# Kernel tuning notes

Measured on AMD Instinct MI355X. Metric: run time of the kernel, lower is better.

Reference implementation:

```python
import jax, jax.numpy as jnp
import numpy as np

N_QUBITS = 8

# Quantum circuit math: starting from |0...0>, apply RX(x_i) then RY(theta_i) on each
# wire independently (product state preserved). Exact PauliZ expectation per wire:
#   RX(x)|0> = cos(x/2)|0> - i sin(x/2)|1>;  after RY(t):
#   <Z> = cos(x) * cos(t)
# This is the exact closed form of the full state-vector simulation the torch module runs.

def setup_inputs() -> dict:
    key = jax.random.key(0)
    k1, k2, k3, k4 = jax.random.split(key, 4)
    B, S, D, F = 4, 4096, 1024, 4096
    x = jax.random.normal(k1, (B, S, D), dtype=jnp.float32)
    theta = jax.random.normal(k2, (N_QUBITS,), dtype=jnp.float32)
    W1 = jax.random.normal(k3, (F, N_QUBITS), dtype=jnp.float32) * (1.0 / np.sqrt(N_QUBITS))
    W2 = jax.random.normal(k4, (D, F), dtype=jnp.float32) * (1.0 / np.sqrt(F))
    return {"x": x, "theta": theta, "W1": W1, "W2": W2}


def reference(x, theta, W1, W2):
    # Encoder only reads the first n_qubits features of each token.
    z = jnp.cos(x[..., :N_QUBITS]) * jnp.cos(theta)          # [B, S, Q] PauliZ expectations
    h = jax.nn.relu(jnp.einsum('bsq,fq->bsf', z, W1))        # [B, S, ffn_dim]
    return jnp.einsum('bsf,df->bsd', h, W2)                  # [B, S, embed_dim]
```

## Files before the change

### kernel.cpp

```cpp
#include <hip/hip_runtime.h>
#include <hip/hip_bf16.h>
#include <math.h>


using f32x4  = __attribute__((ext_vector_type(4))) float;
using bf16x8 = __attribute__((ext_vector_type(8))) short;
using i32x4  = __attribute__((ext_vector_type(4))) int;

#define M_TOT 16384
#define N_TOT 1024
#define K_TOT 4096
#define NKT   128
#define ATB   16384
#define BTB   8192

static const size_t H_BYTES   = (size_t)M_TOT * K_TOT * 2;
static const size_t W2B_BYTES = (size_t)N_TOT * K_TOT * 2;
static const size_t WS_NEED   = H_BYTES + W2B_BYTES;

#define SWZ32(row, bytecol) ((bytecol) ^ ((((row) >> 1) & 3) << 4))

#define GLD16(gp, lp) __builtin_amdgcn_global_load_lds( \
    (const __attribute__((address_space(1))) unsigned int*)(const void*)(gp), \
    (__attribute__((address_space(3))) unsigned int*)(void*)(lp), 16, 0, 0)

static __device__ inline unsigned short f2bf(float f) {
    __hip_bfloat16 b = __float2bfloat16(f);
    unsigned short u;
    __builtin_memcpy(&u, &b, 2);
    return u;
}

__global__ __launch_bounds__(256)
void k_prep(const float* __restrict__ x, const float* __restrict__ theta,
            const float* __restrict__ W1, const float* __restrict__ W2,
            char* __restrict__ hws, char* __restrict__ w2ws)
{
    __shared__ float sZ[256 * 8];
    __shared__ float sW[128 * 8];
    const int tid = threadIdx.x;

    if (blockIdx.x < 2048) {
        const int bx = blockIdx.x >> 5;
        const int by = blockIdx.x & 31;

        {
            const float* xp = x + ((size_t)bx * 256 + tid) * 1024;
            f32x4 a = *reinterpret_cast<const f32x4*>(xp);
            f32x4 b = *reinterpret_cast<const f32x4*>(xp + 4);
            #pragma unroll
            for (int q = 0; q < 4; ++q) {
                sZ[tid * 8 + q]     = cosf(a[q]) * cosf(theta[q]);
                sZ[tid * 8 + 4 + q] = cosf(b[q]) * cosf(theta[q + 4]);
            }
        }
        *reinterpret_cast<f32x4*>(&sW[tid * 4]) =
            *reinterpret_cast<const f32x4*>(W1 + (size_t)by * 1024 + tid * 4);
        __syncthreads();

        const int tm = tid >> 4;
        const int tk = tid & 15;

        f32x4 wA[8], wB[8];
        #pragma unroll
        for (int kk = 0; kk < 8; ++kk) {
            wA[kk] = *reinterpret_cast<const f32x4*>(&sW[(tk * 8 + kk) * 8]);
            wB[kk] = *reinterpret_cast<const f32x4*>(&sW[(tk * 8 + kk) * 8 + 4]);
        }

        const int kt = by * 4 + (tk >> 2);
        const int slotb = (tk & 3) * 16;
        char* tb = hws + ((size_t)(bx * NKT + kt)) * ATB;

        #pragma unroll
        for (int i = 0; i < 16; ++i) {
            const int R = tm * 16 + i;
            f32x4 za = *reinterpret_cast<const f32x4*>(&sZ[R * 8]);
            f32x4 zb = *reinterpret_cast<const f32x4*>(&sZ[R * 8 + 4]);
            unsigned hu[8];
            #pragma unroll
            for (int kk = 0; kk < 8; ++kk) {
                float h = 0.f;
                #pragma unroll
                for (int q = 0; q < 4; ++q) {
                    h = fmaf(za[q], wA[kk][q], h);
                    h = fmaf(zb[q], wB[kk][q], h);
                }
                hu[kk] = (unsigned)f2bf(fmaxf(h, 0.f));
            }
            i32x4 pk;
            pk[0] = (int)(hu[0] | (hu[1] << 16));
            pk[1] = (int)(hu[2] | (hu[3] << 16));
            pk[2] = (int)(hu[4] | (hu[5] << 16));
            pk[3] = (int)(hu[6] | (hu[7] << 16));
            *reinterpret_cast<i32x4*>(tb + R * 64 + SWZ32(R, slotb)) = pk;
        }
    } else {
        const int gt = (blockIdx.x - 2048) * 256 + tid;
        const int n  = gt >> 9;
        const int k8 = gt & 511;
        const float* p = W2 + (size_t)n * K_TOT + k8 * 8;
        f32x4 a = *reinterpret_cast<const f32x4*>(p);
        f32x4 b = *reinterpret_cast<const f32x4*>(p + 4);
        i32x4 pk;
        pk[0] = (int)((unsigned)f2bf(a[0]) | ((unsigned)f2bf(a[1]) << 16));
        pk[1] = (int)((unsigned)f2bf(a[2]) | ((unsigned)f2bf(a[3]) << 16));
        pk[2] = (int)((unsigned)f2bf(b[0]) | ((unsigned)f2bf(b[1]) << 16));
        pk[3] = (int)((unsigned)f2bf(b[2]) | ((unsigned)f2bf(b[3]) << 16));
        const int nt = n >> 7, r = n & 127, kt = k8 >> 2, slotb = (k8 & 3) * 16;
        char* dst = w2ws + ((size_t)(nt * NKT + kt)) * BTB + r * 64 + SWZ32(r, slotb);
        *reinterpret_cast<i32x4*>(dst) = pk;
    }
}


#define STAGE_T(T, RB2) do {                                              \
    const char* ga_ = aT + (size_t)(T) * ATB;                             \
    const char* gb_ = bT + (size_t)(T) * BTB;                             \
    char* la_ = lds + (RB2) * 24576;                                      \
    GLD16(ga_ + tid * 16,         la_ + tid * 16);                        \
    GLD16(ga_ + 4096 + tid * 16,  la_ + 4096 + tid * 16);                 \
    GLD16(ga_ + 8192 + tid * 16,  la_ + 8192 + tid * 16);                 \
    GLD16(ga_ + 12288 + tid * 16, la_ + 12288 + tid * 16);                \
    GLD16(gb_ + tid * 16,         la_ + 16384 + tid * 16);                \
    GLD16(gb_ + 4096 + tid * 16,  la_ + 16384 + 4096 + tid * 16);         \
} while (0)

#define TILE(RB, T, DOSTAGE, WN) do {                                     \
    const char* sa_ = lds + (RB) * 24576;                                 \
    const char* sb_ = sa_ + 16384;                                        \
    bf16x8 af[8], bfr[4];                                                 \
    _Pragma("unroll")                                                     \
    for (int j = 0; j < 4; ++j)                                           \
        bfr[j] = *reinterpret_cast<const bf16x8*>(sb_ + boff[j]);         \
    _Pragma("unroll")                                                     \
    for (int i = 0; i < 4; ++i)                                           \
        af[i] = *reinterpret_cast<const bf16x8*>(sa_ + aoff[i]);          \
    __builtin_amdgcn_sched_barrier(0);                                    \
    _Pragma("unroll")                                                     \
    for (int i = 4; i < 8; ++i)                                           \
        af[i] = *reinterpret_cast<const bf16x8*>(sa_ + aoff[i]);          \
    if (DOSTAGE) STAGE_T((T) + 2, ((RB) + 2) % 3);                        \
    asm volatile("s_waitcnt lgkmcnt(4)" ::: "memory");                    \
    __builtin_amdgcn_sched_barrier(0);                                    \
    __builtin_amdgcn_s_setprio(1);                                        \
    _Pragma("unroll")                                                     \
    for (int i = 0; i < 4; ++i)                                           \
        _Pragma("unroll")                                                 \
        for (int j = 0; j < 4; ++j)                                       \
            acc[i][j] = __builtin_amdgcn_mfma_f32_16x16x32_bf16(af[i], bfr[j], acc[i][j], 0, 0, 0); \
    __builtin_amdgcn_s_setprio(0);                                        \
    asm volatile("s_waitcnt lgkmcnt(0)" ::: "memory");                    \
    __builtin_amdgcn_sched_barrier(0);                                    \
    __builtin_amdgcn_s_setprio(1);                                        \
    _Pragma("unroll")                                                     \
    for (int i = 4; i < 8; ++i)                                           \
        _Pragma("unroll")                                                 \
        for (int j = 0; j < 4; ++j)                                       \
            acc[i][j] = __builtin_amdgcn_mfma_f32_16x16x32_bf16(af[i], bfr[j], acc[i][j], 0, 0, 0); \
    __builtin_amdgcn_s_setprio(0);                                        \
    asm volatile("s_waitcnt vmcnt(" #WN ")" ::: "memory");                \
    __builtin_amdgcn_sched_barrier(0);                                    \
    __builtin_amdgcn_s_barrier();                                         \
    __builtin_amdgcn_sched_barrier(0);                                    \
} while (0)

#define TILE_LAST(RB) do {                                                \
    const char* sa_ = lds + (RB) * 24576;                                 \
    const char* sb_ = sa_ + 16384;                                        \
    bf16x8 af[8], bfr[4];                                                 \
    _Pragma("unroll")                                                     \
    for (int i = 0; i < 8; ++i)                                           \
        af[i] = *reinterpret_cast<const bf16x8*>(sa_ + aoff[i]);          \
    _Pragma("unroll")                                                     \
    for (int j = 0; j < 4; ++j)                                           \
        bfr[j] = *reinterpret_cast<const bf16x8*>(sb_ + boff[j]);         \
    asm volatile("s_waitcnt lgkmcnt(0)" ::: "memory");                    \
    __builtin_amdgcn_sched_barrier(0);                                    \
    _Pragma("unroll")                                                     \
    for (int i = 0; i < 8; ++i)                                           \
        _Pragma("unroll")                                                 \
        for (int j = 0; j < 4; ++j)                                       \
            acc[i][j] = __builtin_amdgcn_mfma_f32_16x16x32_bf16(af[i], bfr[j], acc[i][j], 0, 0, 0); \
} while (0)

__global__ __launch_bounds__(256, 2)
void k_gemm(const char* __restrict__ hws, const char* __restrict__ w2ws,
            float* __restrict__ out)
{
    __shared__ __align__(16) char lds[73728];

    const int tid  = threadIdx.x;
    const int lane = tid & 63;
    const int wave = tid >> 6;
    const int wm = wave >> 1;
    const int wn = wave & 1;

    const int bid  = blockIdx.x;
    const int mtlo = bid & 7;
    const int ntb  = (bid >> 3) & 7;
    const int mt   = ((bid >> 6) << 3) | mtlo;

    const char* aT = hws  + (size_t)mt  * NKT * ATB;
    const char* bT = w2ws + (size_t)ntb * NKT * BTB;

    const int l16 = lane & 15;
    const int sl16 = (lane >> 4) * 16;
    int aoff[8], boff[4];
    #pragma unroll
    for (int i = 0; i < 8; ++i) {
        const int r = wm * 128 + i * 16 + l16;
        aoff[i] = r * 64 + SWZ32(r, sl16);
    }
    #pragma unroll
    for (int j = 0; j < 4; ++j) {
        const int r = wn * 64 + j * 16 + l16;
        boff[j] = r * 64 + SWZ32(r, sl16);
    }

    f32x4 acc[8][4];
    #pragma unroll
    for (int i = 0; i < 8; ++i)
        #pragma unroll
        for (int j = 0; j < 4; ++j)
            acc[i][j] = {0.f, 0.f, 0.f, 0.f};

    STAGE_T(0, 0);
    STAGE_T(1, 1);
    asm volatile("s_waitcnt vmcnt(6)" ::: "memory");
    __builtin_amdgcn_sched_barrier(0);
    __builtin_amdgcn_s_barrier();
    __builtin_amdgcn_sched_barrier(0);

    #pragma unroll 1
    for (int t = 0; t < 126; t += 3) {
        TILE(0, t,     1, 6);
        TILE(1, t + 1, 1, 6);
        TILE(2, t + 2, 1, 6);
    }
    TILE(0, 126, 0, 0);
    TILE_LAST(1);

    const int orow0 = mt * 256 + wm * 128 + (lane >> 4) * 4;
    const int ocol0 = ntb * 128 + wn * 64 + l16;
    #pragma unroll
    for (int i = 0; i < 8; ++i)
        #pragma unroll
        for (int j = 0; j < 4; ++j)
            #pragma unroll
            for (int jj = 0; jj < 4; ++jj)
                out[(size_t)(orow0 + i * 16 + jj) * N_TOT + (ocol0 + j * 16)] = acc[i][j][jj];
}

__global__ __launch_bounds__(256, 3)
void qffn_fused(const float* __restrict__ x, const float* __restrict__ theta,
                const float* __restrict__ W1, const float* __restrict__ W2,
                float* __restrict__ out)
{
    __shared__ __align__(16) unsigned short sA[128 * 64];
    __shared__ __align__(16) unsigned short sB[128 * 64];

    const int tid  = threadIdx.x;
    const int lane = tid & 63;
    const int wave = tid >> 6;
    const int m0 = blockIdx.x * 128;
    const int n0 = blockIdx.y * 128;

    const int arow = tid & 127;
    float zc[8];
    {
        const float* xp = x + (size_t)(m0 + arow) * 1024;
        f32x4 x0 = *reinterpret_cast<const f32x4*>(xp);
        f32x4 x1 = *reinterpret_cast<const f32x4*>(xp + 4);
        #pragma unroll
        for (int q = 0; q < 4; ++q) {
            zc[q]     = cosf(x0[q]) * cosf(theta[q]);
            zc[q + 4] = cosf(x1[q]) * cosf(theta[q + 4]);
        }
    }

    f32x4 acc[4][4];
    #pragma unroll
    for (int i = 0; i < 4; ++i)
        #pragma unroll
        for (int j = 0; j < 4; ++j)
            acc[i][j] = {0.f, 0.f, 0.f, 0.f};

    const int wr  = (wave >> 1) * 64;
    const int wc  = (wave & 1) * 64;
    const int l16 = lane & 15;
    const int lk8 = (lane >> 4) * 8;

    for (int k0 = 0; k0 < K_TOT; k0 += 64) {
        #pragma unroll
        for (int g = 0; g < 4; ++g) {
            const int cg  = (tid >> 7) + 2 * g;
            const int cgu = __builtin_amdgcn_readfirstlane(cg);
            const float* w1p = W1 + (size_t)(k0 + cgu * 8) * 8;
            i32x4 pk;
            #pragma unroll
            for (int p = 0; p < 4; ++p) {
                float h0 = 0.f, h1 = 0.f;
                #pragma unroll
                for (int q = 0; q < 8; ++q) {
                    h0 = fmaf(zc[q], w1p[(2 * p) * 8 + q], h0);
                    h1 = fmaf(zc[q], w1p[(2 * p + 1) * 8 + q], h1);
                }
                pk[p] = (int)(((unsigned)f2bf(fmaxf(h0, 0.f))) |
                              (((unsigned)f2bf(fmaxf(h1, 0.f))) << 16));
            }
            const int off = (arow * 64 + cg * 8) ^ ((arow & 7) << 3);
            *reinterpret_cast<i32x4*>(&sA[off]) = pk;
        }
        {
            const int fi = tid & 15;
            const int rb = tid >> 4;
            #pragma unroll
            for (int r = 0; r < 8; ++r) {
                const int row = rb + r * 16;
                f32x4 v = *(reinterpret_cast<const f32x4*>(W2 + (size_t)(n0 + row) * K_TOT + k0) + fi);
                unsigned p0 = (unsigned)f2bf(v[0]) | ((unsigned)f2bf(v[1]) << 16);
                unsigned p1 = (unsigned)f2bf(v[2]) | ((unsigned)f2bf(v[3]) << 16);
                const int off = (row * 64 + fi * 4) ^ ((row & 7) << 3);
                *reinterpret_cast<unsigned*>(&sB[off])     = p0;
                *reinterpret_cast<unsigned*>(&sB[off + 2]) = p1;
            }
        }
        __syncthreads();

        #pragma unroll
        for (int s = 0; s < 2; ++s) {
            bf16x8 af2[4], bf2[4];
            #pragma unroll
            for (int i = 0; i < 4; ++i) {
                const int row = wr + i * 16 + l16;
                const int off = (row * 64 + s * 32 + lk8) ^ ((row & 7) << 3);
                af2[i] = *reinterpret_cast<const bf16x8*>(&sA[off]);
            }
            #pragma unroll
            for (int j = 0; j < 4; ++j) {
                const int row = wc + j * 16 + l16;
                const int off = (row * 64 + s * 32 + lk8) ^ ((row & 7) << 3);
                bf2[j] = *reinterpret_cast<const bf16x8*>(&sB[off]);
            }
            #pragma unroll
            for (int i = 0; i < 4; ++i)
                #pragma unroll
                for (int j = 0; j < 4; ++j)
                    acc[i][j] = __builtin_amdgcn_mfma_f32_16x16x32_bf16(af2[i], bf2[j], acc[i][j], 0, 0, 0);
        }
        __syncthreads();
    }

    const int orow0 = m0 + wr + (lane >> 4) * 4;
    const int ocol0 = n0 + wc + l16;
    #pragma unroll
    for (int i = 0; i < 4; ++i)
        #pragma unroll
        for (int j = 0; j < 4; ++j)
            #pragma unroll
            for (int jj = 0; jj < 4; ++jj)
                out[(size_t)(orow0 + i * 16 + jj) * N_TOT + (ocol0 + j * 16)] = acc[i][j][jj];
}

extern "C" void kernel_launch(void* const* d_in, const int* in_sizes, int n_in,
                              void* d_out, int out_size, void* d_ws, size_t ws_size,
                              hipStream_t stream) {
    const float* x     = (const float*)d_in[0];
    const float* theta = (const float*)d_in[1];
    const float* W1    = (const float*)d_in[2];
    const float* W2    = (const float*)d_in[3];
    float* out = (float*)d_out;

    if (ws_size >= WS_NEED) {
        char* hws  = (char*)d_ws;
        char* w2ws = (char*)d_ws + H_BYTES;

        k_prep<<<dim3(4096), dim3(256), 0, stream>>>(x, theta, W1, W2, hws, w2ws);
        k_gemm<<<dim3(512), dim3(256), 0, stream>>>(hws, w2ws, out);
    } else {
        qffn_fused<<<dim3(M_TOT / 128, N_TOT / 128), dim3(256), 0, stream>>>(x, theta, W1, W2, out);
    }
}
```

Measured before the change: 147.0 us.

## Load W2 B-fragments directly from global into registers, bypassing LDS

The B operand (bf16 W2 tiles) is now loaded by each wave straight from global memory into a triple-buffered register array instead of being staged through LDS. The W2 workspace layout drops its swizzle so fragments sit contiguously, and the LDS footprint shrinks from 72KB to 48KB. This removes LDS write/read traffic for B and frees shared memory. In exchange it adds 12 bf16x8 registers per thread, which raises register pressure at the 2-waves-per-EU bound, and the B loads are redundant across the two wm waves. The vmcnt waits are raised to account for the extra loads in flight.

```diff
diff --git a/kernel.cpp b/kernel.cpp
--- a/kernel.cpp
+++ b/kernel.cpp
@@ -108,31 +108,32 @@
         pk[2] = (int)((unsigned)f2bf(b[0]) | ((unsigned)f2bf(b[1]) << 16));
         pk[3] = (int)((unsigned)f2bf(b[2]) | ((unsigned)f2bf(b[3]) << 16));
         const int nt = n >> 7, r = n & 127, kt = k8 >> 2, slotb = (k8 & 3) * 16;
-        char* dst = w2ws + ((size_t)(nt * NKT + kt)) * BTB + r * 64 + SWZ32(r, slotb);
+        char* dst = w2ws + ((size_t)(nt * NKT + kt)) * BTB + r * 64 + slotb;
         *reinterpret_cast<i32x4*>(dst) = pk;
     }
 }
 
 
-#define STAGE_T(T, RB2) do {                                              \
+#define STAGE_A(T, RB2) do {                                              \
     const char* ga_ = aT + (size_t)(T) * ATB;                             \
-    const char* gb_ = bT + (size_t)(T) * BTB;                             \
-    char* la_ = lds + (RB2) * 24576;                                      \
+    char* la_ = lds + (RB2) * 16384;                                      \
     GLD16(ga_ + tid * 16,         la_ + tid * 16);                        \
     GLD16(ga_ + 4096 + tid * 16,  la_ + 4096 + tid * 16);                 \
     GLD16(ga_ + 8192 + tid * 16,  la_ + 8192 + tid * 16);                 \
     GLD16(ga_ + 12288 + tid * 16, la_ + 12288 + tid * 16);                \
-    GLD16(gb_ + tid * 16,         la_ + 16384 + tid * 16);                \
-    GLD16(gb_ + 4096 + tid * 16,  la_ + 16384 + 4096 + tid * 16);         \
 } while (0)
 
+#define BLOAD(T1, RD) do {                                                \
+    const char* gb_ = bT + (size_t)(T1) * BTB + boffG;                    \
+    Pb[RD][0] = *reinterpret_cast<const bf16x8*>(gb_);                    \
+    Pb[RD][1] = *reinterpret_cast<const bf16x8*>(gb_ + 1024);             \
+    Pb[RD][2] = *reinterpret_cast<const bf16x8*>(gb_ + 2048);             \
+    Pb[RD][3] = *reinterpret_cast<const bf16x8*>(gb_ + 3072);             \
+} while (0)
+
 #define TILE(RB, T, DOSTAGE, WN) do {                                     \
-    const char* sa_ = lds + (RB) * 24576;                                 \
-    const char* sb_ = sa_ + 16384;                                        \
-    bf16x8 af[8], bfr[4];                                                 \
-    _Pragma("unroll")                                                     \
-    for (int j = 0; j < 4; ++j)                                           \
-        bfr[j] = *reinterpret_cast<const bf16x8*>(sb_ + boff[j]);         \
+    const char* sa_ = lds + (RB) * 16384;                                 \
+    bf16x8 af[8];                                                         \
     _Pragma("unroll")                                                     \
     for (int i = 0; i < 4; ++i)                                           \
         af[i] = *reinterpret_cast<const bf16x8*>(sa_ + aoff[i]);          \
@@ -140,7 +141,10 @@
     _Pragma("unroll")                                                     \
     for (int i = 4; i < 8; ++i)                                           \
         af[i] = *reinterpret_cast<const bf16x8*>(sa_ + aoff[i]);          \
-    if (DOSTAGE) STAGE_T((T) + 2, ((RB) + 2) % 3);                        \
+    if (DOSTAGE) {                                                        \
+        BLOAD((T) + 2, ((RB) + 2) % 3);                                   \
+        STAGE_A((T) + 2, ((RB) + 2) % 3);                                 \
+    }                                                                     \
     asm volatile("s_waitcnt lgkmcnt(4)" ::: "memory");                    \
     __builtin_amdgcn_sched_barrier(0);                                    \
     __builtin_amdgcn_s_setprio(1);                                        \
@@ -148,7 +152,7 @@
     for (int i = 0; i < 4; ++i)                                           \
         _Pragma("unroll")                                                 \
         for (int j = 0; j < 4; ++j)                                       \
-            acc[i][j] = __builtin_amdgcn_mfma_f32_16x16x32_bf16(af[i], bfr[j], acc[i][j], 0, 0, 0); \
+            acc[i][j] = __builtin_amdgcn_mfma_f32_16x16x32_bf16(af[i], Pb[RB][j], acc[i][j], 0, 0, 0); \
     __builtin_amdgcn_s_setprio(0);                                        \
     asm volatile("s_waitcnt lgkmcnt(0)" ::: "memory");                    \
     __builtin_amdgcn_sched_barrier(0);                                    \
@@ -157,7 +161,7 @@
     for (int i = 4; i < 8; ++i)                                           \
         _Pragma("unroll")                                                 \
         for (int j = 0; j < 4; ++j)                                       \
-            acc[i][j] = __builtin_amdgcn_mfma_f32_16x16x32_bf16(af[i], bfr[j], acc[i][j], 0, 0, 0); \
+            acc[i][j] = __builtin_amdgcn_mfma_f32_16x16x32_bf16(af[i], Pb[RB][j], acc[i][j], 0, 0, 0); \
     __builtin_amdgcn_s_setprio(0);                                        \
     asm volatile("s_waitcnt vmcnt(" #WN ")" ::: "memory");                \
     __builtin_amdgcn_sched_barrier(0);                                    \
@@ -166,29 +170,25 @@
 } while (0)
 
 #define TILE_LAST(RB) do {                                                \
-    const char* sa_ = lds + (RB) * 24576;                                 \
-    const char* sb_ = sa_ + 16384;                                        \
-    bf16x8 af[8], bfr[4];                                                 \
+    const char* sa_ = lds + (RB) * 16384;                                 \
+    bf16x8 af[8];                                                         \
     _Pragma("unroll")                                                     \
     for (int i = 0; i < 8; ++i)                                           \
         af[i] = *reinterpret_cast<const bf16x8*>(sa_ + aoff[i]);          \
-    _Pragma("unroll")                                                     \
-    for (int j = 0; j < 4; ++j)                                           \
-        bfr[j] = *reinterpret_cast<const bf16x8*>(sb_ + boff[j]);         \
     asm volatile("s_waitcnt lgkmcnt(0)" ::: "memory");                    \
     __builtin_amdgcn_sched_barrier(0);                                    \
     _Pragma("unroll")                                                     \
     for (int i = 0; i < 8; ++i)                                           \
         _Pragma("unroll")                                                 \
         for (int j = 0; j < 4; ++j)                                       \
-            acc[i][j] = __builtin_amdgcn_mfma_f32_16x16x32_bf16(af[i], bfr[j], acc[i][j], 0, 0, 0); \
+            acc[i][j] = __builtin_amdgcn_mfma_f32_16x16x32_bf16(af[i], Pb[RB][j], acc[i][j], 0, 0, 0); \
 } while (0)
 
 __global__ __launch_bounds__(256, 2)
 void k_gemm(const char* __restrict__ hws, const char* __restrict__ w2ws,
             float* __restrict__ out)
 {
-    __shared__ __align__(16) char lds[73728];
+    __shared__ __align__(16) char lds[49152];
 
     const int tid  = threadIdx.x;
     const int lane = tid & 63;
@@ -206,18 +206,15 @@
 
     const int l16 = lane & 15;
     const int sl16 = (lane >> 4) * 16;
-    int aoff[8], boff[4];
+    int aoff[8];
     #pragma unroll
     for (int i = 0; i < 8; ++i) {
         const int r = wm * 128 + i * 16 + l16;
         aoff[i] = r * 64 + SWZ32(r, sl16);
     }
-    #pragma unroll
-    for (int j = 0; j < 4; ++j) {
-        const int r = wn * 64 + j * 16 + l16;
-        boff[j] = r * 64 + SWZ32(r, sl16);
-    }
-
+    const int boffG = (wn * 64 + l16) * 64 + sl16;
+
+    bf16x8 Pb[3][4];
     f32x4 acc[8][4];
     #pragma unroll
     for (int i = 0; i < 8; ++i)
@@ -225,18 +222,20 @@
         for (int j = 0; j < 4; ++j)
             acc[i][j] = {0.f, 0.f, 0.f, 0.f};
 
-    STAGE_T(0, 0);
-    STAGE_T(1, 1);
-    asm volatile("s_waitcnt vmcnt(6)" ::: "memory");
+    BLOAD(0, 0);
+    STAGE_A(0, 0);
+    BLOAD(1, 1);
+    STAGE_A(1, 1);
+    asm volatile("s_waitcnt vmcnt(8)" ::: "memory");
     __builtin_amdgcn_sched_barrier(0);
     __builtin_amdgcn_s_barrier();
     __builtin_amdgcn_sched_barrier(0);
 
     #pragma unroll 1
     for (int t = 0; t < 126; t += 3) {
-        TILE(0, t,     1, 6);
-        TILE(1, t + 1, 1, 6);
-        TILE(2, t + 2, 1, 6);
+        TILE(0, t,     1, 8);
+        TILE(1, t + 1, 1, 8);
+        TILE(2, t + 2, 1, 8);
     }
     TILE(0, 126, 0, 0);
     TILE_LAST(1);
```

Result: slower. 157.0 us (+6.8%).
